# Kernel optimization log

Measured on AMD Instinct MI355X. Metric: run time of the kernel, lower is better.

Reference implementation:

```python
import jax, jax.numpy as jnp
import numpy as np

C = 8.0


def setup_inputs() -> dict:
    key = jax.random.key(0)
    k1, k2, k3, k4 = jax.random.split(key, 4)
    B, H, W = 16, 512, 512
    grid = jax.random.normal(k1, (B, 2, H, W), jnp.float32)
    u = jax.random.uniform(k2, (B, 2), jnp.float32)
    # dx = -C*x takes both signs (exercise both branches); dy = C*y >= 0 as the
    # original torch slicing requires.
    gt_sym_axis = jnp.stack([u[:, 0] * 2.0 - 1.0, u[:, 1]], axis=-1)
    gd_sym_axis = jax.random.normal(k3, (B, 2), jnp.float32)
    mask = jax.random.uniform(k4, (B, H, W), jnp.float32)
    return {"grid": grid, "gt_sym_axis": gt_sym_axis,
            "gd_sym_axis": gd_sym_axis, "mask": mask}


def _per_item(g, m, dx, dy, sym_x, sym_y):
    # g: (2, H, W) flow grid, m: (H, W) mask; dx, dy, sym_x, sym_y scalars.
    _, h, w = g.shape
    dy1f = jnp.floor(dy); dx1f = jnp.floor(dx)
    dy2f = dy1f + 1.0;    dx2f = dx1f + 1.0
    dy1 = dy1f.astype(jnp.int32); dy2 = dy1 + 1
    dx1 = dx1f.astype(jnp.int32); dx2 = dx1 + 1

    ii = jnp.arange(h)[:, None]   # (H, 1)
    jj = jnp.arange(w)[None, :]   # (1, W)

    def gat(arr, r, c):
        # clipped dynamic gather; invalid region is masked out later
        return arr[..., jnp.clip(r, 0, h - 1), jnp.clip(c, 0, w - 1)]

    wcol = {1: dx2f - dx, 2: dx - dx1f}   # bilinear col weights (dx1 / dx2)
    wrow = {1: dy2f - dy, 2: dy - dy1f}   # bilinear row weights (dy1 / dy2)
    dys = {1: dy1, 2: dy2}
    dxs = {1: dx1, 2: dx2}

    # ---- dx > 0 branch: delta_ba(i,j) = g[i,j] - g[i+dy_a, j+dx_b] ----
    delta_p = jnp.zeros_like(g)
    for b in (1, 2):
        for a in (1, 2):
            delta_p = delta_p + wcol[b] * wrow[a] * (g - gat(g, ii + dys[a], jj + dxs[b]))
    valid_p = ((ii < h - dy2) & (jj < w - dx2)).astype(g.dtype)
    err_p = delta_p[0] * sym_y + delta_p[1] * sym_x
    cnt_p = ((h - dy2) * (w - dx2)).astype(g.dtype)
    loss_p = jnp.sum(m * valid_p * err_p * err_p) / cnt_p

    # ---- dx <= 0 branch: delta_ba(i,j) = g[i+dy2, j+t_b] - g[i+s_a, j+t_b-dx_b] ----
    s = {1: 1, 2: 0}   # row base offset for dy1 / dy2 variant
    t = {1: 0, 2: 1}   # col base offset for dx1 / dx2 variant
    delta_n = jnp.zeros_like(g)
    for b in (1, 2):
        for a in (1, 2):
            first = gat(g, ii + dy2, jj + t[b])
            second = gat(g, ii + s[a], jj + t[b] - dxs[b])
            delta_n = delta_n + wcol[b] * wrow[a] * (first - second)
    valid_n = ((ii < h - dy2) & (jj < w + dx1)).astype(g.dtype)
    m_n = gat(m, ii + dy2, jj - dx1)
    err_n = delta_n[0] * sym_y + delta_n[1] * sym_x
    cnt_n = ((h - dy2) * (w + dx1)).astype(g.dtype)
    loss_n = jnp.sum(m_n * valid_n * err_n * err_n) / cnt_n

    return jnp.where(dx > 0, loss_p, loss_n)


def reference(grid, gt_sym_axis, gd_sym_axis, mask):
    dx = -C * gt_sym_axis[:, 0]
    dy = C * gt_sym_axis[:, 1]
    sym_x = gd_sym_axis[:, 0]
    sym_y = gd_sym_axis[:, 1]
    losses = jax.vmap(_per_item)(grid, mask, dx, dy, sym_x, sym_y)
    return jnp.mean(losses)
```

## Files before the change

### kernel.cpp

```cpp
#include <hip/hip_runtime.h>

#define HH 512
#define WW 512
#define NB 16
#define RPB 8
#define NCHUNK (HH / RPB)
#define NBLOCKS (NB * NCHUNK)

__global__ __launch_bounds__(256) void mbfs_main(
    const float* __restrict__ grid,
    const float* __restrict__ gt,
    const float* __restrict__ gd,
    const float* __restrict__ mask,
    float* __restrict__ partials)
{
    const int b     = blockIdx.y;
    const int chunk = blockIdx.x;
    const int row0  = chunk * RPB;

    const float dx   = -8.0f * gt[2 * b + 0];
    const float dy   =  8.0f * gt[2 * b + 1];
    const float symx = gd[2 * b + 0];
    const float symy = gd[2 * b + 1];

    const float dy1f = floorf(dy);
    const float dx1f = floorf(dx);
    const int dy1 = (int)dy1f;
    const int dx1 = (int)dx1f;
    const int dy2 = dy1 + 1;
    const int dx2 = dx1 + 1;
    const float wc1 = (dx1f + 1.0f) - dx;
    const float wc2 = dx - dx1f;
    const float wr1 = (dy1f + 1.0f) - dy;
    const float wr2 = dy - dy1f;

    const float* g0 = grid + (size_t)b * 2 * HH * WW;
    const float* g1 = g0 + HH * WW;
    const float* mk = mask + (size_t)b * HH * WW;

    const int imax = HH - dy2;
    const int rsub = threadIdx.x >> 7;
    const int j0   = (threadIdx.x & 127) << 2;
    const int rend = min(row0 + RPB, imax);

    float acc = 0.0f;
    float cnt;

    if (dx > 0.0f) {
        const int jmax = WW - dx2;
        cnt = (float)imax * (float)jmax;
        for (int i = row0 + rsub; i < rend; i += 2) {
            const float* gc0 = g0 + i * WW;
            const float* gc1 = g1 + i * WW;
            const float* ga0 = g0 + (i + dy1) * WW;
            const float* gb0 = g0 + (i + dy2) * WW;
            const float* ga1 = g1 + (i + dy1) * WW;
            const float* gb1 = g1 + (i + dy2) * WW;
            const float* mr  = mk + i * WW;

            const float4 c0 = *(const float4*)(gc0 + j0);
            const float4 c1 = *(const float4*)(gc1 + j0);
            const float4 mv = *(const float4*)(mr + j0);

            float z0[5], z1[5];
            #pragma unroll
            for (int k = 0; k < 5; ++k) {
                int col = j0 + dx1 + k;
                col = min(col, WW - 1);
                z0[k] = wr1 * ga0[col] + wr2 * gb0[col];
                z1[k] = wr1 * ga1[col] + wr2 * gb1[col];
            }
            const float cc0[4] = {c0.x, c0.y, c0.z, c0.w};
            const float cc1[4] = {c1.x, c1.y, c1.z, c1.w};
            const float mm[4]  = {mv.x, mv.y, mv.z, mv.w};
            #pragma unroll
            for (int k = 0; k < 4; ++k) {
                float s0 = wc1 * z0[k] + wc2 * z0[k + 1];
                float s1 = wc1 * z1[k] + wc2 * z1[k + 1];
                float d0 = cc0[k] - s0;
                float d1 = cc1[k] - s1;
                float e  = d0 * symy + d1 * symx;
                float w  = (j0 + k < jmax) ? mm[k] : 0.0f;
                acc += w * e * e;
            }
        }
    } else {
        const int a    = -dx1;
        const int jmax = WW + dx1;
        cnt = (float)imax * (float)jmax;
        for (int i = row0 + rsub; i < rend; i += 2) {
            const float* r20  = g0 + (i + dy2) * WW;
            const float* r21  = g1 + (i + dy2) * WW;
            const float* ri0  = g0 + i * WW;
            const float* ri10 = g0 + (i + 1) * WW;
            const float* ri1  = g1 + i * WW;
            const float* ri11 = g1 + (i + 1) * WW;
            const float* mr   = mk + (i + dy2) * WW;

            const float4 h0 = *(const float4*)(r20 + j0);
            const float4 h1 = *(const float4*)(r21 + j0);
            const int je = min(j0 + 4, WW - 1);
            const float h0e = r20[je];
            const float h1e = r21[je];

            float zn0[4], zn1[4], mm[4];
            #pragma unroll
            for (int k = 0; k < 4; ++k) {
                int jm = min(j0 + k + a, WW - 1);
                zn0[k] = wr1 * ri10[jm] + wr2 * ri0[jm];
                zn1[k] = wr1 * ri11[jm] + wr2 * ri1[jm];
                mm[k]  = mr[jm];
            }
            const float hh0[5] = {h0.x, h0.y, h0.z, h0.w, h0e};
            const float hh1[5] = {h1.x, h1.y, h1.z, h1.w, h1e};
            #pragma unroll
            for (int k = 0; k < 4; ++k) {
                float d0 = wc1 * hh0[k] + wc2 * hh0[k + 1] - zn0[k];
                float d1 = wc1 * hh1[k] + wc2 * hh1[k + 1] - zn1[k];
                float e  = d0 * symy + d1 * symx;
                float w  = (j0 + k < jmax) ? mm[k] : 0.0f;
                acc += w * e * e;
            }
        }
    }

    #pragma unroll
    for (int off = 32; off > 0; off >>= 1)
        acc += __shfl_down(acc, off, 64);
    __shared__ float part[4];
    const int lane = threadIdx.x & 63;
    const int wv   = threadIdx.x >> 6;
    if (lane == 0) part[wv] = acc;
    __syncthreads();
    if (threadIdx.x == 0) {
        float s = part[0] + part[1] + part[2] + part[3];
        partials[b * NCHUNK + chunk] = s / (cnt * (float)NB);
    }
}

__global__ __launch_bounds__(256) void mbfs_reduce(
    const float* __restrict__ partials, float* __restrict__ out)
{
    float v = 0.0f;
    for (int idx = threadIdx.x; idx < NBLOCKS; idx += 256) v += partials[idx];
    #pragma unroll
    for (int off = 32; off > 0; off >>= 1)
        v += __shfl_down(v, off, 64);
    __shared__ float part[4];
    const int lane = threadIdx.x & 63;
    const int wv   = threadIdx.x >> 6;
    if (lane == 0) part[wv] = v;
    __syncthreads();
    if (threadIdx.x == 0) out[0] = part[0] + part[1] + part[2] + part[3];
}

extern "C" void kernel_launch(void* const* d_in, const int* in_sizes, int n_in,
                              void* d_out, int out_size, void* d_ws, size_t ws_size,
                              hipStream_t stream) {
    const float* grid_p = (const float*)d_in[0];
    const float* gt_p   = (const float*)d_in[1];
    const float* gd_p   = (const float*)d_in[2];
    const float* mask_p = (const float*)d_in[3];
    float* out_p = (float*)d_out;
    float* ws_p  = (float*)d_ws;

    dim3 g(NCHUNK, NB);
    mbfs_main<<<g, 256, 0, stream>>>(grid_p, gt_p, gd_p, mask_p, ws_p);
    mbfs_reduce<<<1, 256, 0, stream>>>(ws_p, out_p);
}
```

Measured before the change: 100.6 us.

## Stage shifted rows in swizzled LDS and reindex negative-dx branch

Each block now handles two output rows and first stages the shifted grid rows into shared memory with a bank-conflict-avoiding swizzle, then reads the unaligned column-shifted taps from LDS instead of scattered global loads. The dx<=0 branch is reindexed over the shifted output position, so global loads become aligned float4 and only the LDS reads are misaligned. Blocks grow from 64 to 256 per batch and the per-block row loop is dropped. In exchange there is an extra barrier, LDS traffic, and redundant staging of overlapping rows between neighbouring blocks.

```diff
diff --git a/kernel.cpp b/kernel.cpp
--- a/kernel.cpp
+++ b/kernel.cpp
@@ -3,9 +3,11 @@
 #define HH 512
 #define WW 512
 #define NB 16
-#define RPB 8
-#define NCHUNK (HH / RPB)
+#define NRB 2
+#define NCHUNK (HH / NRB)
 #define NBLOCKS (NB * NCHUNK)
+
+__device__ __forceinline__ int swz(int c) { return ((c & 3) << 7) | (c >> 2); }
 
 __global__ __launch_bounds__(256) void mbfs_main(
     const float* __restrict__ grid,
@@ -14,9 +16,14 @@
     const float* __restrict__ mask,
     float* __restrict__ partials)
 {
-    const int b     = blockIdx.y;
-    const int chunk = blockIdx.x;
-    const int row0  = chunk * RPB;
+    __shared__ float lds[6 * 512];
+
+    const int b    = blockIdx.y;
+    const int i0   = blockIdx.x * NRB;
+    const int tid  = threadIdx.x;
+    const int rsub = tid >> 7;
+    const int jt   = tid & 127;
+    const int j0   = jt << 2;
 
     const float dx   = -8.0f * gt[2 * b + 0];
     const float dy   =  8.0f * gt[2 * b + 1];
@@ -39,48 +46,58 @@
     const float* mk = mask + (size_t)b * HH * WW;
 
     const int imax = HH - dy2;
-    const int rsub = threadIdx.x >> 7;
-    const int j0   = (threadIdx.x & 127) << 2;
-    const int rend = min(row0 + RPB, imax);
-
     float acc = 0.0f;
     float cnt;
 
     if (dx > 0.0f) {
         const int jmax = WW - dx2;
         cnt = (float)imax * (float)jmax;
-        for (int i = row0 + rsub; i < rend; i += 2) {
-            const float* gc0 = g0 + i * WW;
-            const float* gc1 = g1 + i * WW;
-            const float* ga0 = g0 + (i + dy1) * WW;
-            const float* gb0 = g0 + (i + dy2) * WW;
-            const float* ga1 = g1 + (i + dy1) * WW;
-            const float* gb1 = g1 + (i + dy2) * WW;
-            const float* mr  = mk + i * WW;
-
-            const float4 c0 = *(const float4*)(gc0 + j0);
-            const float4 c1 = *(const float4*)(gc1 + j0);
-            const float4 mv = *(const float4*)(mr + j0);
+
+        for (int t = tid; t < 6 * 128; t += 256) {
+            const int s  = t >> 7;
+            const int f  = t & 127;
+            const int c  = f << 2;
+            const int rr = (s < 3) ? s : s - 3;
+            const float* gp = (s < 3) ? g0 : g1;
+            int ir = min(i0 + dy1 + rr, HH - 1);
+            const float4 v = *(const float4*)(gp + ir * WW + c);
+            float* L = lds + s * 512;
+            L[swz(c)]     = v.x;
+            L[swz(c + 1)] = v.y;
+            L[swz(c + 2)] = v.z;
+            L[swz(c + 3)] = v.w;
+        }
+        __syncthreads();
+
+        const int i = i0 + rsub;
+        if (i < imax) {
+            const float4 c0 = *(const float4*)(g0 + i * WW + j0);
+            const float4 c1 = *(const float4*)(g1 + i * WW + j0);
+            const float4 mv = *(const float4*)(mk + i * WW + j0);
+            const float* A0 = lds + rsub * 512;
+            const float* B0 = lds + (rsub + 1) * 512;
+            const float* A1 = lds + (3 + rsub) * 512;
+            const float* B1 = lds + (4 + rsub) * 512;
 
             float z0[5], z1[5];
             #pragma unroll
             for (int k = 0; k < 5; ++k) {
-                int col = j0 + dx1 + k;
-                col = min(col, WW - 1);
-                z0[k] = wr1 * ga0[col] + wr2 * gb0[col];
-                z1[k] = wr1 * ga1[col] + wr2 * gb1[col];
+                const int c  = min(j0 + dx1 + k, WW - 1);
+                const int sc = swz(c);
+                z0[k] = wr1 * A0[sc] + wr2 * B0[sc];
+                z1[k] = wr1 * A1[sc] + wr2 * B1[sc];
             }
             const float cc0[4] = {c0.x, c0.y, c0.z, c0.w};
             const float cc1[4] = {c1.x, c1.y, c1.z, c1.w};
             const float mm[4]  = {mv.x, mv.y, mv.z, mv.w};
             #pragma unroll
             for (int k = 0; k < 4; ++k) {
-                float s0 = wc1 * z0[k] + wc2 * z0[k + 1];
-                float s1 = wc1 * z1[k] + wc2 * z1[k + 1];
-                float d0 = cc0[k] - s0;
-                float d1 = cc1[k] - s1;
-                float e  = d0 * symy + d1 * symx;
-                float w  = (j0 + k < jmax) ? mm[k] : 0.0f;
+                const float s0 = wc1 * z0[k] + wc2 * z0[k + 1];
+                const float s1 = wc1 * z1[k] + wc2 * z1[k + 1];
+                const float d0 = cc0[k] - s0;
+                const float d1 = cc1[k] - s1;
+                const float e  = d0 * symy + d1 * symx;
+                const float w  = (j0 + k < jmax) ? mm[k] : 0.0f;
                 acc += w * e * e;
             }
         }
@@ -88,37 +105,55 @@
         const int a    = -dx1;
         const int jmax = WW + dx1;
         cnt = (float)imax * (float)jmax;
-        for (int i = row0 + rsub; i < rend; i += 2) {
-            const float* r20  = g0 + (i + dy2) * WW;
-            const float* r21  = g1 + (i + dy2) * WW;
-            const float* ri0  = g0 + i * WW;
-            const float* ri10 = g0 + (i + 1) * WW;
-            const float* ri1  = g1 + i * WW;
-            const float* ri11 = g1 + (i + 1) * WW;
-            const float* mr   = mk + (i + dy2) * WW;
-
-            const float4 h0 = *(const float4*)(r20 + j0);
-            const float4 h1 = *(const float4*)(r21 + j0);
-            const int je = min(j0 + 4, WW - 1);
-            const float h0e = r20[je];
-            const float h1e = r21[je];
-
-            float zn0[4], zn1[4], mm[4];
+
+        for (int t = tid; t < 4 * 128; t += 256) {
+            const int s  = t >> 7;
+            const int f  = t & 127;
+            const int c  = f << 2;
+            const int rr = s & 1;
+            const float* gp = (s < 2) ? g0 : g1;
+            int ir = min(i0 + dy2 + rr, HH - 1);
+            const float4 v = *(const float4*)(gp + ir * WW + c);
+            float* L = lds + s * 512;
+            L[swz(c)]     = v.x;
+            L[swz(c + 1)] = v.y;
+            L[swz(c + 2)] = v.z;
+            L[swz(c + 3)] = v.w;
+        }
+        __syncthreads();
+
+        const int i = i0 + rsub;
+        if (i < imax) {
+            const float4 p00 = *(const float4*)(g0 + i * WW + j0);
+            const float4 p01 = *(const float4*)(g0 + (i + 1) * WW + j0);
+            const float4 p10 = *(const float4*)(g1 + i * WW + j0);
+            const float4 p11 = *(const float4*)(g1 + (i + 1) * WW + j0);
+            const float4 mv  = *(const float4*)(mk + (i + dy2) * WW + j0);
+            const float* H0 = lds + rsub * 512;
+            const float* H1 = lds + (2 + rsub) * 512;
+
+            float hh0[5], hh1[5];
+            #pragma unroll
+            for (int k = 0; k < 5; ++k) {
+                int c = j0 - a + k;
+                c = max(0, min(c, WW - 1));
+                const int sc = swz(c);
+                hh0[k] = H0[sc];
+                hh1[k] = H1[sc];
+            }
+            const float q00[4] = {p00.x, p00.y, p00.z, p00.w};
+            const float q01[4] = {p01.x, p01.y, p01.z, p01.w};
+            const float q10[4] = {p10.x, p10.y, p10.z, p10.w};
+            const float q11[4] = {p11.x, p11.y, p11.z, p11.w};
+            const float mm[4]  = {mv.x, mv.y, mv.z, mv.w};
             #pragma unroll
             for (int k = 0; k < 4; ++k) {
-                int jm = min(j0 + k + a, WW - 1);
-                zn0[k] = wr1 * ri10[jm] + wr2 * ri0[jm];
-                zn1[k] = wr1 * ri11[jm] + wr2 * ri1[jm];
-                mm[k]  = mr[jm];
-            }
-            const float hh0[5] = {h0.x, h0.y, h0.z, h0.w, h0e};
-            const float hh1[5] = {h1.x, h1.y, h1.z, h1.w, h1e};
-            #pragma unroll
-            for (int k = 0; k < 4; ++k) {
-                float d0 = wc1 * hh0[k] + wc2 * hh0[k + 1] - zn0[k];
-                float d1 = wc1 * hh1[k] + wc2 * hh1[k + 1] - zn1[k];
-                float e  = d0 * symy + d1 * symx;
-                float w  = (j0 + k < jmax) ? mm[k] : 0.0f;
+                const float zn0 = wr1 * q01[k] + wr2 * q00[k];
+                const float zn1 = wr1 * q11[k] + wr2 * q10[k];
+                const float d0  = wc1 * hh0[k] + wc2 * hh0[k + 1] - zn0;
+                const float d1  = wc1 * hh1[k] + wc2 * hh1[k + 1] - zn1;
+                const float e   = d0 * symy + d1 * symx;
+                const float w   = (j0 + k >= a) ? mm[k] : 0.0f;
                 acc += w * e * e;
             }
         }
@@ -128,13 +163,13 @@
     for (int off = 32; off > 0; off >>= 1)
         acc += __shfl_down(acc, off, 64);
     __shared__ float part[4];
-    const int lane = threadIdx.x & 63;
-    const int wv   = threadIdx.x >> 6;
+    const int lane = tid & 63;
+    const int wv   = tid >> 6;
     if (lane == 0) part[wv] = acc;
     __syncthreads();
-    if (threadIdx.x == 0) {
-        float s = part[0] + part[1] + part[2] + part[3];
-        partials[b * NCHUNK + chunk] = s / (cnt * (float)NB);
+    if (tid == 0) {
+        const float s = part[0] + part[1] + part[2] + part[3];
+        partials[b * NCHUNK + blockIdx.x] = s / (cnt * (float)NB);
     }
 }
 
```

Result: faster. 97.61 us (-3.0%).
